# Performance work log

Hardware: AMD Instinct MI355X
Metric: run time of the kernel (lower is better)

The kernel has to match this reference:

```python
import jax, jax.numpy as jnp
import numpy as np

NEG_INF = jnp.float32(-1e30)
EPS = 1e-7  # keras.backend.ctc_batch_cost epsilon


def ctc_batch_cost(y_true, y_pred):
    """Faithful CTC loss (keras ctc_batch_cost semantics): y_pred are
    probabilities [B,T,C], blank = C-1, full input/label lengths.
    Returns per-example negative log likelihood [B,1]."""
    B, T, C = y_pred.shape
    L = y_true.shape[1]
    S = 2 * L + 1  # extended label length (blanks interleaved)
    blank = C - 1

    log_probs = jnp.log(y_pred + EPS)  # [B,T,C]

    # Extended label sequence: blank, l0, blank, l1, ..., blank  -> [B,S]
    ext = jnp.full((B, S), blank, dtype=y_true.dtype)
    ext = ext.at[:, 1::2].set(y_true)

    # Skip transition allowed at s if ext[s] != blank and ext[s] != ext[s-2]
    skip = jnp.concatenate(
        [jnp.zeros((B, 2), dtype=bool),
         (ext[:, 2:] != blank) & (ext[:, 2:] != ext[:, :-2])], axis=1)  # [B,S]

    # Gather log-probs of extended labels per timestep: [T,B,S]
    lp_ext = jnp.take_along_axis(log_probs, ext[:, None, :], axis=2)  # [B,T,S]
    lp_ext = jnp.transpose(lp_ext, (1, 0, 2))  # [T,B,S]

    # alpha init at t=0: only positions 0 (blank) and 1 (first label)
    alpha0 = jnp.full((B, S), NEG_INF, dtype=log_probs.dtype)
    alpha0 = alpha0.at[:, 0].set(lp_ext[0, :, 0])
    alpha0 = alpha0.at[:, 1].set(lp_ext[0, :, 1])

    pad1 = jnp.full((B, 1), NEG_INF, dtype=log_probs.dtype)
    pad2 = jnp.full((B, 2), NEG_INF, dtype=log_probs.dtype)

    def step(alpha, lp_t):
        a_stay = alpha
        a_prev = jnp.concatenate([pad1, alpha[:, :-1]], axis=1)
        a_skip = jnp.where(skip, jnp.concatenate([pad2, alpha[:, :-2]], axis=1), NEG_INF)
        m = jnp.maximum(jnp.maximum(a_stay, a_prev), a_skip)
        lse = m + jnp.log(jnp.exp(a_stay - m) + jnp.exp(a_prev - m) + jnp.exp(a_skip - m))
        return lse + lp_t, None

    alpha_T, _ = jax.lax.scan(step, alpha0, lp_ext[1:])  # [B,S]

    # log P = logsumexp over last blank and last label positions
    end = jnp.stack([alpha_T[:, S - 1], alpha_T[:, S - 2]], axis=1)  # [B,2]
    loglik = jax.nn.logsumexp(end, axis=1)  # [B]
    return -loglik[:, None]  # [B,1] like keras ctc_batch_cost


def setup_inputs() -> dict:
    key = jax.random.key(0)
    k1, k2 = jax.random.split(key)
    B, T, C, L = 512, 512, 128, 32
    y_true = jax.random.randint(k1, (B, L), 0, C - 1, dtype=jnp.int64 if jax.config.read('jax_enable_x64') else jnp.int32)
    y_pred = jax.random.uniform(k2, (B, T, C), dtype=jnp.float32)
    return {"y_true": y_true, "y_pred": y_pred}


def reference(y_true, y_pred):
    return ctc_batch_cost(y_true, y_pred)
```

## Files before the change

kernel.cpp:

```cpp
#include <hip/hip_runtime.h>


#define EPSF 1e-7f

constexpr int T_ = 512;
constexpr int C_ = 128;
constexpr int L_ = 32;
constexpr int NF = 17;
constexpr int NB = 28;

__launch_bounds__(64)
__global__ void ctc_loss_kernel(const int* __restrict__ y_true,
                                const float* __restrict__ y_pred,
                                float* __restrict__ out) {
    const int bidx = blockIdx.x;
    const int lane = threadIdx.x;

    const float* bb  = y_pred + (size_t)bidx * T_ * C_;
    const int*   lbl = y_true + bidx * L_;

    int   cf[7];
    float sg[7];
    float msk[9];
#pragma unroll
    for (int i = 0; i < 7; ++i) {
        const int v = lane - i;
        int c = C_ - 1; float s = 0.f;
        if (v >= 1 && (v & 1)) {
            c = lbl[(v - 1) >> 1];
            if (v >= 3 && c != lbl[((v - 1) >> 1) - 1]) s = 1.f;
        }
        cf[i] = c * 4; sg[i] = s;
    }
#pragma unroll
    for (int i = 0; i < 9; ++i) msk[i] = (lane >= i) ? 1.f : 0.f;

    int   cb[9];
    float gd[7];
    float mdn[9];
#pragma unroll
    for (int i = 0; i < 9; ++i) {
        const int u = lane + 1 + i;
        int c = C_ - 1;
        if (u <= 64 && (u & 1)) c = lbl[(u - 1) >> 1];
        cb[i] = c * 4;
        mdn[i] = (lane + i <= 63) ? 1.f : 0.f;
    }
#pragma unroll
    for (int i = 0; i < 7; ++i) {
        const int v = lane + i + 3;
        float g = 0.f;
        if (v <= 64 && (v & 1) && lbl[(v - 1) >> 1] != lbl[((v - 1) >> 1) - 1]) g = 1.f;
        gd[i] = g;
    }

    auto gat = [](const float* r, int boff) -> float {
        return *(const float*)((const char*)r + boff);
    };

    float a   = (lane < 2) ? (gat(bb, cf[0]) + EPSF) : 0.f;
    float a64 = 0.f;
    float b   = (lane >= 62) ? 1.f : 0.f;
    float b0  = 0.f;
    int ef = 0, eb = 0;

    float Qf[3][NF];
    float Qb[3][NB];

    auto loadqf = [&](float (&Qk)[NF], const float* r) {
        Qk[0]  = gat(r, cf[0]);          Qk[1]  = gat(r, cf[1]);
        Qk[2]  = gat(r, cf[2]);          Qk[3]  = gat(r, cf[3]);
        Qk[4]  = gat(r, cf[4]);          Qk[5]  = gat(r, cf[5]);
        Qk[6]  = gat(r, cf[6]);
        Qk[7]  = gat(r + C_, cf[0]);     Qk[8]  = gat(r + C_, cf[1]);
        Qk[9]  = gat(r + C_, cf[2]);     Qk[10] = gat(r + C_, cf[3]);
        Qk[11] = gat(r + C_, cf[4]);
        Qk[12] = gat(r + 2*C_, cf[0]);   Qk[13] = gat(r + 2*C_, cf[1]);
        Qk[14] = gat(r + 2*C_, cf[2]);
        Qk[15] = gat(r + 3*C_, cf[0]);   Qk[16] = gat(r + 3*C_, cf[1]);
    };
    auto loadqb = [&](float (&Qk)[NB], const float* r3) {
        const float* r2 = r3 - C_;
        const float* r1 = r3 - 2*C_;
        const float* r0 = r3 - 3*C_;
#pragma unroll
        for (int i = 0; i < 9; ++i) Qk[i]      = gat(r3, cb[i]);
#pragma unroll
        for (int i = 0; i < 7; ++i) Qk[9 + i]  = gat(r2, cb[i]);
#pragma unroll
        for (int i = 0; i < 5; ++i) Qk[16 + i] = gat(r1, cb[i]);
#pragma unroll
        for (int i = 0; i < 3; ++i) Qk[21 + i] = gat(r0, cb[i]);
        Qk[24] = r3[C_ - 1]; Qk[25] = r2[C_ - 1];
        Qk[26] = r1[C_ - 1]; Qk[27] = r0[C_ - 1];
    };

    auto fgroup4 = [&](float (&Qk)[NF]) {
        float A[9];
        A[0] = a;
#pragma unroll
        for (int i = 1; i <= 8; ++i) A[i] = __shfl_up(a, i) * msk[i];
        float B[7];
#pragma unroll
        for (int i = 0; i <= 6; ++i)
            B[i] = (A[i] + A[i + 1] + sg[i] * A[i + 2]) * (Qk[i] + EPSF);
        float Cc[5];
#pragma unroll
        for (int i = 0; i <= 4; ++i)
            Cc[i] = (B[i] + B[i + 1] + sg[i] * B[i + 2]) * (Qk[7 + i] + EPSF);
        float D[3];
#pragma unroll
        for (int i = 0; i <= 2; ++i)
            D[i] = (Cc[i] + Cc[i + 1] + sg[i] * Cc[i + 2]) * (Qk[12 + i] + EPSF);
        float z = a64;
        z = (z + A[0])  * (Qk[1]  + EPSF);
        z = (z + B[0])  * (Qk[8]  + EPSF);
        z = (z + Cc[0]) * (Qk[13] + EPSF);
        z = (z + D[0])  * (Qk[16] + EPSF);
        a64 = z;
        a = (D[0] + D[1] + sg[0] * D[2]) * (Qk[15] + EPSF);
    };

    auto bgroup4 = [&](float (&Qk)[NB]) {
        float BA[9];
        BA[0] = b;
#pragma unroll
        for (int i = 1; i <= 8; ++i) BA[i] = __shfl_down(b, i) * mdn[i];
        float G[9];
#pragma unroll
        for (int i = 0; i <= 8; ++i) G[i] = BA[i] * (Qk[i] + EPSF);
        float X[7];
#pragma unroll
        for (int i = 0; i <= 6; ++i) X[i] = G[i] + G[i + 1] + gd[i] * G[i + 2];
        float G2[7];
#pragma unroll
        for (int i = 0; i <= 6; ++i) G2[i] = X[i] * (Qk[9 + i] + EPSF);
        float X2[5];
#pragma unroll
        for (int i = 0; i <= 4; ++i) X2[i] = G2[i] + G2[i + 1] + gd[i] * G2[i + 2];
        float G3[5];
#pragma unroll
        for (int i = 0; i <= 4; ++i) G3[i] = X2[i] * (Qk[16 + i] + EPSF);
        float X3[3];
#pragma unroll
        for (int i = 0; i <= 2; ++i) X3[i] = G3[i] + G3[i + 1] + gd[i] * G3[i + 2];
        float G4[3];
#pragma unroll
        for (int i = 0; i <= 2; ++i) G4[i] = X3[i] * (Qk[21 + i] + EPSF);
        float z = b0;
        z = (Qk[24] + EPSF) * z + G[0];
        z = (Qk[25] + EPSF) * z + G2[0];
        z = (Qk[26] + EPSF) * z + G3[0];
        z = (Qk[27] + EPSF) * z + G4[0];
        b0 = z;
        b = G4[0] + G4[1] + gd[0] * G4[2];
    };

    float smpF[16], smpB[16];
    auto sampleF = [&]() {
#pragma unroll
        for (int i = 0; i < 16; ++i) smpF[i] = __shfl(a, 4 * i + 3);
    };
    auto sampleB = [&]() {
#pragma unroll
        for (int i = 0; i < 16; ++i) smpB[i] = __shfl(b, 4 * i + 3);
    };
    auto apply = [&](const float* s, float& x, float& y, int& e) {
        float t[8];
#pragma unroll
        for (int i = 0; i < 8; ++i) t[i] = fmaxf(s[i], s[i + 8]);
#pragma unroll
        for (int i = 0; i < 4; ++i) t[i] = fmaxf(t[i], t[i + 4]);
        float m = fmaxf(fmaxf(t[0], t[1]), fmaxf(t[2], t[3]));
        m = fmaxf(m, 9.094947e-13f);
        int be = (int)(__float_as_uint(m) >> 23);
        be = (be < 67) ? 67 : ((be > 187) ? 187 : be);
        e += be - 127;
        const float inv = __uint_as_float((unsigned)(254 - be) << 23);
        x *= inv; y *= inv;
    };

#pragma unroll
    for (int k = 0; k < 3; ++k) {
        loadqf(Qf[k], bb + (size_t)(1 + 4 * k) * C_);
        loadqb(Qb[k], bb + (size_t)(511 - 4 * k) * C_);
    }
    sampleF(); sampleB();

    for (int i0 = 0; i0 < 63; i0 += 3) {
#pragma unroll
        for (int k = 0; k < 3; ++k) {
            const int t = i0 + k;
            fgroup4(Qf[k]);
            bgroup4(Qb[k]);
            if ((t & 1) == 0) { apply(smpF, a, a64, ef); sampleF(); }
            else              { apply(smpB, b, b0, eb); sampleB(); }
            const int gf = (t + 3 <= 63) ? (t + 3) : 63;
            const int gb = (t + 3 <= 62) ? (t + 3) : 62;
            loadqf(Qf[k], bb + (size_t)(1 + 4 * gf) * C_);
            loadqb(Qb[k], bb + (size_t)(511 - 4 * gb) * C_);
        }
    }

    float qs[12];
#pragma unroll
    for (int r = 0; r < 3; ++r) {
        const float* row = bb + (size_t)(259 - r) * C_;
        qs[4 * r + 0] = gat(row, cb[0]);
        qs[4 * r + 1] = gat(row, cb[1]);
        qs[4 * r + 2] = gat(row, cb[2]);
        qs[4 * r + 3] = row[C_ - 1];
    }

    fgroup4(Qf[0]);
    apply(smpF, a, a64, ef);

#pragma unroll
    for (int r = 0; r < 3; ++r) {
        const float g0  = b * (qs[4 * r + 0] + EPSF);
        const float ba1 = __shfl_down(b, 1) * mdn[1];
        const float ba2 = __shfl_down(b, 2) * mdn[2];
        const float g1  = ba1 * (qs[4 * r + 1] + EPSF);
        const float g2  = ba2 * (qs[4 * r + 2] + EPSF);
        b0 = (qs[4 * r + 3] + EPSF) * b0 + g0;
        b  = g0 + g1 + gd[0] * g2;
    }

    const float NEGB = -1e30f;
    auto lg = [&](float v) -> float { return (v > 0.f) ? __logf(v) : NEGB; };
    const float la   = lg(a);
    const float lb   = lg(b);
    const float ladn = __shfl_down(la, 1);
    float t1 = (lane <= 62) ? (ladn + lb) : NEGB;
    float t2 = NEGB;
    if (lane == 0)  t2 = la + lg(b0);
    if (lane == 63) t2 = lg(a64) + lb;

    float wmax = fmaxf(t1, t2);
#pragma unroll
    for (int off = 1; off < 64; off <<= 1) wmax = fmaxf(wmax, __shfl_xor(wmax, off));

    const float e1 = (t1 > -1e29f) ? __expf(t1 - wmax) : 0.f;
    const float e2 = (t2 > -1e29f) ? __expf(t2 - wmax) : 0.f;
    float p = e1 + e2;
#pragma unroll
    for (int off = 1; off < 64; off <<= 1) p += __shfl_xor(p, off);

    if (lane == 0) {
        const float ll = wmax + __logf(p) + (float)(ef + eb) * 0.6931471805599453f;
        out[bidx] = -ll;
    }
}

extern "C" void kernel_launch(void* const* d_in, const int* in_sizes, int n_in,
                              void* d_out, int out_size, void* d_ws, size_t ws_size,
                              hipStream_t stream) {
    const int*   y_true = (const int*)d_in[0];
    const float* y_pred = (const float*)d_in[1];
    float*       out    = (float*)d_out;

    const int B = out_size;
    ctc_loss_kernel<<<B, 64, 0, stream>>>(y_true, y_pred, out);
}
```

Measured before the change: 226.5 us.

## Split forward and backward CTC chains into separate blocks with atomic-flag merge

Instead of one wavefront per example running both the forward and backward alpha/beta chains interleaved, the kernel launches 2B blocks. Each block runs only one direction and writes its partial state to workspace, and the second block to finish, detected through an atomic counter, combines the two. Per-lane gathers are cut to one column index, with neighbour probabilities fetched by cross-lane shuffles instead of separate gathers. This doubles parallelism and shortens each wave's dependent chain, at the cost of a memset, workspace traffic, extra shuffle work, and fence/atomic synchronization.

```diff
diff --git a/kernel.cpp b/kernel.cpp
--- a/kernel.cpp
+++ b/kernel.cpp
@@ -2,253 +2,280 @@
 
 
 #define EPSF 1e-7f
+#define NEGB (-1e30f)
 
 constexpr int T_ = 512;
 constexpr int C_ = 128;
 constexpr int L_ = 32;
-constexpr int NF = 17;
-constexpr int NB = 28;
+
+__device__ __forceinline__ float gatb(const float* r, int boff) {
+    return *(const float*)((const char*)r + boff);
+}
+
+__device__ __forceinline__ void apply_scale(const float* s, float& x, float& y, int& e) {
+    float t[8];
+#pragma unroll
+    for (int i = 0; i < 8; ++i) t[i] = fmaxf(s[i], s[i + 8]);
+#pragma unroll
+    for (int i = 0; i < 4; ++i) t[i] = fmaxf(t[i], t[i + 4]);
+    float m = fmaxf(fmaxf(t[0], t[1]), fmaxf(t[2], t[3]));
+    m = fmaxf(m, 9.094947e-13f);
+    int be = (int)(__float_as_uint(m) >> 23);
+    be = (be < 67) ? 67 : ((be > 187) ? 187 : be);
+    e += be - 127;
+    const float inv = __uint_as_float((unsigned)(254 - be) << 23);
+    x *= inv; y *= inv;
+}
 
 __launch_bounds__(64)
-__global__ void ctc_loss_kernel(const int* __restrict__ y_true,
-                                const float* __restrict__ y_pred,
-                                float* __restrict__ out) {
-    const int bidx = blockIdx.x;
+__global__ void ctc_chain_kernel(const int* __restrict__ y_true,
+                                 const float* __restrict__ y_pred,
+                                 float* __restrict__ out,
+                                 float* __restrict__ data,
+                                 int* __restrict__ flags,
+                                 int B) {
+    const int blk  = blockIdx.x;
+    const bool fwd = (blk < B);
+    const int bidx = fwd ? blk : blk - B;
     const int lane = threadIdx.x;
-
     const float* bb  = y_pred + (size_t)bidx * T_ * C_;
     const int*   lbl = y_true + bidx * L_;
-
-    int   cf[7];
-    float sg[7];
-    float msk[9];
-#pragma unroll
-    for (int i = 0; i < 7; ++i) {
-        const int v = lane - i;
-        int c = C_ - 1; float s = 0.f;
-        if (v >= 1 && (v & 1)) {
-            c = lbl[(v - 1) >> 1];
-            if (v >= 3 && c != lbl[((v - 1) >> 1) - 1]) s = 1.f;
-        }
-        cf[i] = c * 4; sg[i] = s;
+    float* rec = data + (size_t)bidx * 132;
+
+    if (fwd) {
+        int cf0;
+        {
+            int c = C_ - 1;
+            if (lane & 1) c = lbl[(lane - 1) >> 1];
+            cf0 = c * 4;
+        }
+        float sg[7], msk[9];
+#pragma unroll
+        for (int i = 0; i < 7; ++i) {
+            const int v = lane - i;
+            float s = 0.f;
+            if (v >= 3 && (v & 1) && lbl[(v - 1) >> 1] != lbl[((v - 1) >> 1) - 1]) s = 1.f;
+            sg[i] = s;
+        }
+#pragma unroll
+        for (int i = 0; i < 9; ++i) msk[i] = (lane >= i) ? 1.f : 0.f;
+
+        float a   = (lane < 2) ? (gatb(bb, cf0) + EPSF) : 0.f;
+        float a64 = 0.f;
+        int   ef  = 0;
+        float smp[16];
+        float r0[4], r1[4], r2[4], e0[17], e1[17];
+
+        auto loadg = [&](float (&rv)[4], int g) {
+            const float* base = bb + (size_t)(1 + 4 * g) * C_;
+#pragma unroll
+            for (int j = 0; j < 4; ++j) rv[j] = gatb(base + (size_t)j * C_, cf0);
+        };
+        auto expand = [&](const float (&rv)[4], float (&e)[17]) {
+            e[0] = rv[0];
+#pragma unroll
+            for (int i = 1; i <= 6; ++i) e[i] = __shfl_up(rv[0], i);
+            e[7] = rv[1];
+#pragma unroll
+            for (int i = 1; i <= 4; ++i) e[7 + i] = __shfl_up(rv[1], i);
+            e[12] = rv[2];
+            e[13] = __shfl_up(rv[2], 1);
+            e[14] = __shfl_up(rv[2], 2);
+            e[15] = rv[3];
+            e[16] = __shfl_up(rv[3], 1);
+        };
+        auto sample = [&]() {
+#pragma unroll
+            for (int i = 0; i < 16; ++i) smp[i] = __shfl(a, 4 * i + 3);
+        };
+        auto fgroup4 = [&](const float (&Qk)[17]) {
+            float A[9];
+            A[0] = a;
+#pragma unroll
+            for (int i = 1; i <= 8; ++i) A[i] = __shfl_up(a, i) * msk[i];
+            float Bt[7];
+#pragma unroll
+            for (int i = 0; i <= 6; ++i)
+                Bt[i] = (A[i] + A[i + 1] + sg[i] * A[i + 2]) * (Qk[i] + EPSF);
+            float Cc[5];
+#pragma unroll
+            for (int i = 0; i <= 4; ++i)
+                Cc[i] = (Bt[i] + Bt[i + 1] + sg[i] * Bt[i + 2]) * (Qk[7 + i] + EPSF);
+            float D[3];
+#pragma unroll
+            for (int i = 0; i <= 2; ++i)
+                D[i] = (Cc[i] + Cc[i + 1] + sg[i] * Cc[i + 2]) * (Qk[12 + i] + EPSF);
+            float z = a64;
+            z = (z + A[0])  * (Qk[1]  + EPSF);
+            z = (z + Bt[0]) * (Qk[8]  + EPSF);
+            z = (z + Cc[0]) * (Qk[13] + EPSF);
+            z = (z + D[0])  * (Qk[16] + EPSF);
+            a64 = z;
+            a = (D[0] + D[1] + sg[0] * D[2]) * (Qk[15] + EPSF);
+        };
+
+        loadg(r0, 0); loadg(r1, 1); loadg(r2, 2);
+        expand(r0, e0);
+        sample();
+        for (int t0 = 0; t0 < 60; t0 += 6) {
+            fgroup4(e0); sample();                     expand(r1, e1); loadg(r0, t0 + 3);
+            fgroup4(e1); apply_scale(smp, a, a64, ef); expand(r2, e0); loadg(r1, t0 + 4);
+            fgroup4(e0); sample();                     expand(r0, e1); loadg(r2, t0 + 5);
+            fgroup4(e1); apply_scale(smp, a, a64, ef); expand(r1, e0); loadg(r0, t0 + 6);
+            fgroup4(e0); sample();                     expand(r2, e1); loadg(r1, t0 + 7);
+            fgroup4(e1); apply_scale(smp, a, a64, ef); expand(r0, e0); loadg(r2, t0 + 8);
+        }
+        fgroup4(e0); sample();                     expand(r1, e1); loadg(r0, 63);
+        fgroup4(e1); apply_scale(smp, a, a64, ef); expand(r2, e0);
+        fgroup4(e0); sample();                     expand(r0, e1);
+        fgroup4(e1); apply_scale(smp, a, a64, ef);
+
+        rec[lane] = a;
+        if (lane == 63) rec[64] = a64;
+        if (lane == 0)  rec[65] = (float)ef;
+    } else {
+        int cb0;
+        {
+            const int u = lane + 1;
+            int c = C_ - 1;
+            if (u & 1) c = lbl[(u - 1) >> 1];
+            cb0 = c * 4;
+        }
+        float gd[7], mdn[9];
+#pragma unroll
+        for (int i = 0; i < 9; ++i) mdn[i] = (lane + i <= 63) ? 1.f : 0.f;
+#pragma unroll
+        for (int i = 0; i < 7; ++i) {
+            const int v = lane + i + 3;
+            float g = 0.f;
+            if (v <= 64 && (v & 1) && lbl[(v - 1) >> 1] != lbl[((v - 1) >> 1) - 1]) g = 1.f;
+            gd[i] = g;
+        }
+        float b  = (lane >= 62) ? 1.f : 0.f;
+        float b0 = 0.f;
+        int   eb = 0;
+        float smp[16];
+        float r0[4], r1[4], r2[4], e0[28], e1[28];
+
+        auto loadg = [&](float (&rv)[4], int g) {
+            const float* r3 = bb + (size_t)(511 - 4 * g) * C_;
+#pragma unroll
+            for (int j = 0; j < 4; ++j) rv[j] = gatb(r3 - (size_t)j * C_, cb0);
+        };
+        auto expand = [&](const float (&rv)[4], float (&e)[28]) {
+            e[0] = rv[0];
+#pragma unroll
+            for (int i = 1; i <= 8; ++i) e[i] = __shfl_down(rv[0], i);
+            e[9] = rv[1];
+#pragma unroll
+            for (int i = 1; i <= 6; ++i) e[9 + i] = __shfl_down(rv[1], i);
+            e[16] = rv[2];
+#pragma unroll
+            for (int i = 1; i <= 4; ++i) e[16 + i] = __shfl_down(rv[2], i);
+            e[21] = rv[3];
+            e[22] = __shfl_down(rv[3], 1);
+            e[23] = __shfl_down(rv[3], 2);
+            e[24] = __shfl(rv[0], 63);
+            e[25] = __shfl(rv[1], 63);
+            e[26] = __shfl(rv[2], 63);
+            e[27] = __shfl(rv[3], 63);
+        };
+        auto sample = [&]() {
+#pragma unroll
+            for (int i = 0; i < 16; ++i) smp[i] = __shfl(b, 4 * i + 3);
+        };
+        auto bgroup4 = [&](const float (&Qk)[28]) {
+            float BA[9];
+            BA[0] = b;
+#pragma unroll
+            for (int i = 1; i <= 8; ++i) BA[i] = __shfl_down(b, i) * mdn[i];
+            float G[9];
+#pragma unroll
+            for (int i = 0; i <= 8; ++i) G[i] = BA[i] * (Qk[i] + EPSF);
+            float X[7];
+#pragma unroll
+            for (int i = 0; i <= 6; ++i) X[i] = G[i] + G[i + 1] + gd[i] * G[i + 2];
+            float G2[7];
+#pragma unroll
+            for (int i = 0; i <= 6; ++i) G2[i] = X[i] * (Qk[9 + i] + EPSF);
+            float X2[5];
+#pragma unroll
+            for (int i = 0; i <= 4; ++i) X2[i] = G2[i] + G2[i + 1] + gd[i] * G2[i + 2];
+            float G3[5];
+#pragma unroll
+            for (int i = 0; i <= 4; ++i) G3[i] = X2[i] * (Qk[16 + i] + EPSF);
+            float X3[3];
+#pragma unroll
+            for (int i = 0; i <= 2; ++i) X3[i] = G3[i] + G3[i + 1] + gd[i] * G3[i + 2];
+            float G4[3];
+#pragma unroll
+            for (int i = 0; i <= 2; ++i) G4[i] = X3[i] * (Qk[21 + i] + EPSF);
+            float z = b0;
+            z = (Qk[24] + EPSF) * z + G[0];
+            z = (Qk[25] + EPSF) * z + G2[0];
+            z = (Qk[26] + EPSF) * z + G3[0];
+            z = (Qk[27] + EPSF) * z + G4[0];
+            b0 = z;
+            b = G4[0] + G4[1] + gd[0] * G4[2];
+        };
+
+        loadg(r0, 0); loadg(r1, 1); loadg(r2, 2);
+        expand(r0, e0);
+        sample();
+        for (int t0 = 0; t0 < 60; t0 += 6) {
+            bgroup4(e0); sample();                    expand(r1, e1); loadg(r0, t0 + 3);
+            bgroup4(e1); apply_scale(smp, b, b0, eb); expand(r2, e0); loadg(r1, t0 + 4);
+            bgroup4(e0); sample();                    expand(r0, e1); loadg(r2, t0 + 5);
+            bgroup4(e1); apply_scale(smp, b, b0, eb); expand(r1, e0); loadg(r0, t0 + 6);
+            bgroup4(e0); sample();                    expand(r2, e1); loadg(r1, t0 + 7);
+            bgroup4(e1); apply_scale(smp, b, b0, eb); expand(r0, e0); loadg(r2, t0 + 8);
+        }
+        bgroup4(e0); sample();                    expand(r1, e1);
+        bgroup4(e1); apply_scale(smp, b, b0, eb); expand(r2, e0);
+        bgroup4(e0);
+        float qv[3];
+        qv[0] = gatb(bb + (size_t)259 * C_, cb0);
+        qv[1] = gatb(bb + (size_t)258 * C_, cb0);
+        qv[2] = gatb(bb + (size_t)257 * C_, cb0);
+#pragma unroll
+        for (int r = 0; r < 3; ++r) {
+            const float q0 = qv[r] + EPSF;
+            const float q1 = __shfl_down(qv[r], 1) + EPSF;
+            const float q2 = __shfl_down(qv[r], 2) + EPSF;
+            const float qb = __shfl(qv[r], 63) + EPSF;
+            const float g0 = b * q0;
+            const float g1 = __shfl_down(b, 1) * mdn[1] * q1;
+            const float g2 = __shfl_down(b, 2) * mdn[2] * q2;
+            b0 = qb * b0 + g0;
+            b  = g0 + g1 + gd[0] * g2;
+        }
+
+        rec[66 + lane + 1] = b;
+        if (lane == 0) { rec[66] = b0; rec[66 + 65] = (float)eb; }
     }
-#pragma unroll
-    for (int i = 0; i < 9; ++i) msk[i] = (lane >= i) ? 1.f : 0.f;
-
-    int   cb[9];
-    float gd[7];
-    float mdn[9];
-#pragma unroll
-    for (int i = 0; i < 9; ++i) {
-        const int u = lane + 1 + i;
-        int c = C_ - 1;
-        if (u <= 64 && (u & 1)) c = lbl[(u - 1) >> 1];
-        cb[i] = c * 4;
-        mdn[i] = (lane + i <= 63) ? 1.f : 0.f;
-    }
-#pragma unroll
-    for (int i = 0; i < 7; ++i) {
-        const int v = lane + i + 3;
-        float g = 0.f;
-        if (v <= 64 && (v & 1) && lbl[(v - 1) >> 1] != lbl[((v - 1) >> 1) - 1]) g = 1.f;
-        gd[i] = g;
-    }
-
-    auto gat = [](const float* r, int boff) -> float {
-        return *(const float*)((const char*)r + boff);
-    };
-
-    float a   = (lane < 2) ? (gat(bb, cf[0]) + EPSF) : 0.f;
-    float a64 = 0.f;
-    float b   = (lane >= 62) ? 1.f : 0.f;
-    float b0  = 0.f;
-    int ef = 0, eb = 0;
-
-    float Qf[3][NF];
-    float Qb[3][NB];
-
-    auto loadqf = [&](float (&Qk)[NF], const float* r) {
-        Qk[0]  = gat(r, cf[0]);          Qk[1]  = gat(r, cf[1]);
-        Qk[2]  = gat(r, cf[2]);          Qk[3]  = gat(r, cf[3]);
-        Qk[4]  = gat(r, cf[4]);          Qk[5]  = gat(r, cf[5]);
-        Qk[6]  = gat(r, cf[6]);
-        Qk[7]  = gat(r + C_, cf[0]);     Qk[8]  = gat(r + C_, cf[1]);
-        Qk[9]  = gat(r + C_, cf[2]);     Qk[10] = gat(r + C_, cf[3]);
-        Qk[11] = gat(r + C_, cf[4]);
-        Qk[12] = gat(r + 2*C_, cf[0]);   Qk[13] = gat(r + 2*C_, cf[1]);
-        Qk[14] = gat(r + 2*C_, cf[2]);
-        Qk[15] = gat(r + 3*C_, cf[0]);   Qk[16] = gat(r + 3*C_, cf[1]);
-    };
-    auto loadqb = [&](float (&Qk)[NB], const float* r3) {
-        const float* r2 = r3 - C_;
-        const float* r1 = r3 - 2*C_;
-        const float* r0 = r3 - 3*C_;
-#pragma unroll
-        for (int i = 0; i < 9; ++i) Qk[i]      = gat(r3, cb[i]);
-#pragma unroll
-        for (int i = 0; i < 7; ++i) Qk[9 + i]  = gat(r2, cb[i]);
-#pragma unroll
-        for (int i = 0; i < 5; ++i) Qk[16 + i] = gat(r1, cb[i]);
-#pragma unroll
-        for (int i = 0; i < 3; ++i) Qk[21 + i] = gat(r0, cb[i]);
-        Qk[24] = r3[C_ - 1]; Qk[25] = r2[C_ - 1];
-        Qk[26] = r1[C_ - 1]; Qk[27] = r0[C_ - 1];
-    };
-
-    auto fgroup4 = [&](float (&Qk)[NF]) {
-        float A[9];
-        A[0] = a;
-#pragma unroll
-        for (int i = 1; i <= 8; ++i) A[i] = __shfl_up(a, i) * msk[i];
-        float B[7];
-#pragma unroll
-        for (int i = 0; i <= 6; ++i)
-            B[i] = (A[i] + A[i + 1] + sg[i] * A[i + 2]) * (Qk[i] + EPSF);
-        float Cc[5];
-#pragma unroll
-        for (int i = 0; i <= 4; ++i)
-            Cc[i] = (B[i] + B[i + 1] + sg[i] * B[i + 2]) * (Qk[7 + i] + EPSF);
-        float D[3];
-#pragma unroll
-        for (int i = 0; i <= 2; ++i)
-            D[i] = (Cc[i] + Cc[i + 1] + sg[i] * Cc[i + 2]) * (Qk[12 + i] + EPSF);
-        float z = a64;
-        z = (z + A[0])  * (Qk[1]  + EPSF);
-        z = (z + B[0])  * (Qk[8]  + EPSF);
-        z = (z + Cc[0]) * (Qk[13] + EPSF);
-        z = (z + D[0])  * (Qk[16] + EPSF);
-        a64 = z;
-        a = (D[0] + D[1] + sg[0] * D[2]) * (Qk[15] + EPSF);
-    };
-
-    auto bgroup4 = [&](float (&Qk)[NB]) {
-        float BA[9];
-        BA[0] = b;
-#pragma unroll
-        for (int i = 1; i <= 8; ++i) BA[i] = __shfl_down(b, i) * mdn[i];
-        float G[9];
-#pragma unroll
-        for (int i = 0; i <= 8; ++i) G[i] = BA[i] * (Qk[i] + EPSF);
-        float X[7];
-#pragma unroll
-        for (int i = 0; i <= 6; ++i) X[i] = G[i] + G[i + 1] + gd[i] * G[i + 2];
-        float G2[7];
-#pragma unroll
-        for (int i = 0; i <= 6; ++i) G2[i] = X[i] * (Qk[9 + i] + EPSF);
-        float X2[5];
-#pragma unroll
-        for (int i = 0; i <= 4; ++i) X2[i] = G2[i] + G2[i + 1] + gd[i] * G2[i + 2];
-        float G3[5];
-#pragma unroll
-        for (int i = 0; i <= 4; ++i) G3[i] = X2[i] * (Qk[16 + i] + EPSF);
-        float X3[3];
-#pragma unroll
-        for (int i = 0; i <= 2; ++i) X3[i] = G3[i] + G3[i + 1] + gd[i] * G3[i + 2];
-        float G4[3];
-#pragma unroll
-        for (int i = 0; i <= 2; ++i) G4[i] = X3[i] * (Qk[21 + i] + EPSF);
-        float z = b0;
-        z = (Qk[24] + EPSF) * z + G[0];
-        z = (Qk[25] + EPSF) * z + G2[0];
-        z = (Qk[26] + EPSF) * z + G3[0];
-        z = (Qk[27] + EPSF) * z + G4[0];
-        b0 = z;
-        b = G4[0] + G4[1] + gd[0] * G4[2];
-    };
-
-    float smpF[16], smpB[16];
-    auto sampleF = [&]() {
-#pragma unroll
-        for (int i = 0; i < 16; ++i) smpF[i] = __shfl(a, 4 * i + 3);
-    };
-    auto sampleB = [&]() {
-#pragma unroll
-        for (int i = 0; i < 16; ++i) smpB[i] = __shfl(b, 4 * i + 3);
-    };
-    auto apply = [&](const float* s, float& x, float& y, int& e) {
-        float t[8];
-#pragma unroll
-        for (int i = 0; i < 8; ++i) t[i] = fmaxf(s[i], s[i + 8]);
-#pragma unroll
-        for (int i = 0; i < 4; ++i) t[i] = fmaxf(t[i], t[i + 4]);
-        float m = fmaxf(fmaxf(t[0], t[1]), fmaxf(t[2], t[3]));
-        m = fmaxf(m, 9.094947e-13f);
-        int be = (int)(__float_as_uint(m) >> 23);
-        be = (be < 67) ? 67 : ((be > 187) ? 187 : be);
-        e += be - 127;
-        const float inv = __uint_as_float((unsigned)(254 - be) << 23);
-        x *= inv; y *= inv;
-    };
-
-#pragma unroll
-    for (int k = 0; k < 3; ++k) {
-        loadqf(Qf[k], bb + (size_t)(1 + 4 * k) * C_);
-        loadqb(Qb[k], bb + (size_t)(511 - 4 * k) * C_);
-    }
-    sampleF(); sampleB();
-
-    for (int i0 = 0; i0 < 63; i0 += 3) {
-#pragma unroll
-        for (int k = 0; k < 3; ++k) {
-            const int t = i0 + k;
-            fgroup4(Qf[k]);
-            bgroup4(Qb[k]);
-            if ((t & 1) == 0) { apply(smpF, a, a64, ef); sampleF(); }
-            else              { apply(smpB, b, b0, eb); sampleB(); }
-            const int gf = (t + 3 <= 63) ? (t + 3) : 63;
-            const int gb = (t + 3 <= 62) ? (t + 3) : 62;
-            loadqf(Qf[k], bb + (size_t)(1 + 4 * gf) * C_);
-            loadqb(Qb[k], bb + (size_t)(511 - 4 * gb) * C_);
-        }
-    }
-
-    float qs[12];
-#pragma unroll
-    for (int r = 0; r < 3; ++r) {
-        const float* row = bb + (size_t)(259 - r) * C_;
-        qs[4 * r + 0] = gat(row, cb[0]);
-        qs[4 * r + 1] = gat(row, cb[1]);
-        qs[4 * r + 2] = gat(row, cb[2]);
-        qs[4 * r + 3] = row[C_ - 1];
-    }
-
-    fgroup4(Qf[0]);
-    apply(smpF, a, a64, ef);
-
-#pragma unroll
-    for (int r = 0; r < 3; ++r) {
-        const float g0  = b * (qs[4 * r + 0] + EPSF);
-        const float ba1 = __shfl_down(b, 1) * mdn[1];
-        const float ba2 = __shfl_down(b, 2) * mdn[2];
-        const float g1  = ba1 * (qs[4 * r + 1] + EPSF);
-        const float g2  = ba2 * (qs[4 * r + 2] + EPSF);
-        b0 = (qs[4 * r + 3] + EPSF) * b0 + g0;
-        b  = g0 + g1 + gd[0] * g2;
-    }
-
-    const float NEGB = -1e30f;
-    auto lg = [&](float v) -> float { return (v > 0.f) ? __logf(v) : NEGB; };
-    const float la   = lg(a);
-    const float lb   = lg(b);
-    const float ladn = __shfl_down(la, 1);
-    float t1 = (lane <= 62) ? (ladn + lb) : NEGB;
-    float t2 = NEGB;
-    if (lane == 0)  t2 = la + lg(b0);
-    if (lane == 63) t2 = lg(a64) + lb;
-
-    float wmax = fmaxf(t1, t2);
-#pragma unroll
-    for (int off = 1; off < 64; off <<= 1) wmax = fmaxf(wmax, __shfl_xor(wmax, off));
-
-    const float e1 = (t1 > -1e29f) ? __expf(t1 - wmax) : 0.f;
-    const float e2 = (t2 > -1e29f) ? __expf(t2 - wmax) : 0.f;
-    float p = e1 + e2;
-#pragma unroll
-    for (int off = 1; off < 64; off <<= 1) p += __shfl_xor(p, off);
-
-    if (lane == 0) {
-        const float ll = wmax + __logf(p) + (float)(ef + eb) * 0.6931471805599453f;
-        out[bidx] = -ll;
+
+    __threadfence();
+    int old = 0;
+    if (lane == 0) old = atomicAdd(&flags[bidx], 1);
+    old = __shfl(old, 0);
+    if (old == 1) {
+        __threadfence();
+        const float* Av = data + (size_t)bidx * 132;
+        const float* Bv = Av + 66;
+        auto lg = [](float v) { return (v > 0.f) ? __logf(v) : NEGB; };
+        float t1 = lg(Av[lane]) + lg(Bv[lane]);
+        float t2 = (lane == 63) ? (lg(Av[64]) + lg(Bv[64])) : NEGB;
+        float wmax = fmaxf(t1, t2);
+#pragma unroll
+        for (int off = 1; off < 64; off <<= 1) wmax = fmaxf(wmax, __shfl_xor(wmax, off));
+        float p = ((t1 > -1e29f) ? __expf(t1 - wmax) : 0.f)
+                + ((t2 > -1e29f) ? __expf(t2 - wmax) : 0.f);
+#pragma unroll
+        for (int off = 1; off < 64; off <<= 1) p += __shfl_xor(p, off);
+        if (lane == 0) {
+            const float esum = Av[65] + Bv[65];
+            out[bidx] = -(wmax + __logf(p) + esum * 0.6931471805599453f);
+        }
     }
 }
 
@@ -258,7 +285,11 @@
     const int*   y_true = (const int*)d_in[0];
     const float* y_pred = (const float*)d_in[1];
     float*       out    = (float*)d_out;
-
     const int B = out_size;
-    ctc_loss_kernel<<<B, 64, 0, stream>>>(y_true, y_pred, out);
-}
+
+    int*   flags = (int*)d_ws;
+    float* data  = (float*)((char*)d_ws + 4096);
+
+    hipMemsetAsync(flags, 0, B * sizeof(int), stream);
+    ctc_chain_kernel<<<2 * B, 64, 0, stream>>>(y_true, y_pred, out, data, flags, B);
+}
```

After: 241.4 us. 1.07x slower.
